# Optimization experiments

Measured on AMD Instinct MI355X. Metric: run time of the kernel, lower is better.

## Reference

```python
import jax, jax.numpy as jnp
import numpy as np

N_EXAMPLES = 10  # hardcoded repeat_interleave(10) in the source

def setup_inputs() -> dict:
    key = jax.random.key(0)
    k1, k2, k3, k4 = jax.random.split(key, 4)
    B, L, S, H = 8, 256, 512, 1024
    return {
        "output": jax.random.normal(k1, (B * N_EXAMPLES, L, H), dtype=jnp.float32),
        "context0": jax.random.normal(k2, (B * N_EXAMPLES, L, H), dtype=jnp.float32),
        "context1": jax.random.normal(k3, (B, S, H), dtype=jnp.float32),
        "mask": jnp.zeros((B * N_EXAMPLES, L), dtype=bool),
        "W_out": jax.random.normal(k4, (H, 3 * H), dtype=jnp.float32) * 0.02,
        "b_out": jnp.zeros((H,), dtype=jnp.float32),
    }

def reference(output, context0, context1, mask, W_out, b_out):
    # output, context0: [B*10, L, H]; context1: [B, S, H]
    # NOTE: in the torch source, `attn.data.masked_fill(mask, -inf)` is NOT
    # in-place and its result is discarded, so the mask has no effect on the
    # math. We reproduce that faithfully: `mask` is unused.
    del mask
    set_ctx = jnp.repeat(context1, N_EXAMPLES, axis=0)  # [B*10, S, H]
    # example-attention branch: bmm -> softmax -> bmm
    ex_attn = jax.nn.softmax(jnp.einsum('bld,bsd->bls', output, context0), axis=-1)  # [B*10, L, L]
    # set-attention branch: bmm -> softmax -> bmm
    set_attn = jax.nn.softmax(jnp.einsum('bld,bsd->bls', output, set_ctx), axis=-1)  # [B*10, L, S]
    ex_c = jnp.einsum('bls,bsd->bld', ex_attn, context0)   # [B*10, L, H]
    set_c = jnp.einsum('bls,bsd->bld', set_attn, set_ctx)  # [B*10, L, H]
    all_info = jnp.concatenate([output, ex_c, set_c], axis=-1)  # [B*10, L, 3H]
    out = jnp.tanh(jnp.einsum('blk,hk->blh', all_info, W_out) + b_out)  # [B*10, L, H]
    return (out, ex_attn, set_attn)
```

## Files before the change

kernel.cpp:

```cpp
#include <hip/hip_runtime.h>
#include <stdint.h>
#include <math.h>

typedef unsigned short u16;
typedef __attribute__((ext_vector_type(8))) short short8;
typedef __attribute__((ext_vector_type(4))) float floatx4;

__device__ __forceinline__ u16 f32_to_bf16(float f) {
    union { float f; uint32_t u; } v; v.f = f;
    uint32_t r = v.u + 0x7FFF + ((v.u >> 16) & 1);
    return (u16)(r >> 16);
}
__device__ __forceinline__ float bf16_to_f32(u16 h) {
    union { uint32_t u; float f; } v; v.u = ((uint32_t)h) << 16; return v.f;
}

__device__ __forceinline__ void gl_lds16(const u16* g, u16* l) {
    __builtin_amdgcn_global_load_lds(
        (const __attribute__((address_space(1))) void*)g,
        (__attribute__((address_space(3))) void*)l, 16, 0, 0);
}


__global__ void split_kernel(const float4* __restrict__ x, ushort4* __restrict__ hi,
                             ushort4* __restrict__ lo, long n4) {
    long i = (long)blockIdx.x * blockDim.x + threadIdx.x;
    if (i >= n4) return;
    float4 v = x[i];
    ushort4 h, l;
    h.x = f32_to_bf16(v.x); l.x = f32_to_bf16(v.x - bf16_to_f32(h.x));
    h.y = f32_to_bf16(v.y); l.y = f32_to_bf16(v.y - bf16_to_f32(h.y));
    h.z = f32_to_bf16(v.z); l.z = f32_to_bf16(v.z - bf16_to_f32(h.z));
    h.w = f32_to_bf16(v.w); l.w = f32_to_bf16(v.w - bf16_to_f32(h.w));
    hi[i] = h; lo[i] = l;
}

__global__ void conv_kernel(const float4* __restrict__ x, ushort4* __restrict__ hi, long n4) {
    long i = (long)blockIdx.x * blockDim.x + threadIdx.x;
    if (i >= n4) return;
    float4 v = x[i];
    ushort4 h;
    h.x = f32_to_bf16(v.x); h.y = f32_to_bf16(v.y);
    h.z = f32_to_bf16(v.z); h.w = f32_to_bf16(v.w);
    hi[i] = h;
}

__global__ void transpose_bf16(const float* __restrict__ src, u16* __restrict__ dst,
                               int R, int C) {
    __shared__ float tile[32][33];
    long base = (long)blockIdx.z * R * C;
    int c0 = blockIdx.x * 32, r0 = blockIdx.y * 32;
    #pragma unroll
    for (int i = threadIdx.y; i < 32; i += 8)
        tile[i][threadIdx.x] = src[base + (long)(r0 + i) * C + c0 + threadIdx.x];
    __syncthreads();
    #pragma unroll
    for (int i = threadIdx.y; i < 32; i += 8)
        dst[base + (long)(c0 + i) * R + r0 + threadIdx.x] = f32_to_bf16(tile[threadIdx.x][i]);
}

template <int VPT>
__global__ void softmax_rows(float* __restrict__ data, u16* __restrict__ outb) {
    const int SL = VPT * 64;
    int row = blockIdx.x * 4 + (threadIdx.x >> 6);
    int lane = threadIdx.x & 63;
    long base = (long)row * SL + lane;
    float v[VPT];
    #pragma unroll
    for (int i = 0; i < VPT; ++i) v[i] = data[base + i * 64];
    float m = v[0];
    #pragma unroll
    for (int i = 1; i < VPT; ++i) m = fmaxf(m, v[i]);
    #pragma unroll
    for (int off = 32; off > 0; off >>= 1) m = fmaxf(m, __shfl_xor(m, off, 64));
    float s = 0.f;
    #pragma unroll
    for (int i = 0; i < VPT; ++i) { v[i] = __expf(v[i] - m); s += v[i]; }
    #pragma unroll
    for (int off = 32; off > 0; off >>= 1) s += __shfl_xor(s, off, 64);
    float inv = 1.0f / s;
    #pragma unroll
    for (int i = 0; i < VPT; ++i) {
        float r = v[i] * inv;
        data[base + i * 64] = r;
        outb[base + i * 64] = f32_to_bf16(r);
    }
}

struct GemmP {
    const u16* A[3];
    const u16* B[3];
    long strideAb, strideBb, strideCb;
    int bdiv, nseg, Kper, lda, ldb, ldc, mode;
    float* Cf; u16* Cb; const float* bias;
};

__global__ __launch_bounds__(256) void gemm_bt(GemmP p) {
    __shared__ u16 As[128 * 64];
    __shared__ u16 Bs[128 * 64];
    const int tid  = threadIdx.x;
    const int lane = tid & 63;
    const int wave = tid >> 6;
    const int quad = lane >> 4;
    const int l15  = lane & 15;
    const int wm = (wave & 1) * 64;
    const int wn = (wave >> 1) * 64;
    const int n0 = blockIdx.x * 128;
    const int m0 = blockIdx.y * 128;
    const int bz = blockIdx.z;

    const int stg_r8 = tid >> 3;
    const int stg_c  = ((tid & 7) ^ (stg_r8 & 7)) * 8;
    const int xorl   = l15 & 7;

    floatx4 acc[4][4];
    #pragma unroll
    for (int i = 0; i < 4; ++i)
        #pragma unroll
        for (int j = 0; j < 4; ++j)
            acc[i][j] = (floatx4){0.f, 0.f, 0.f, 0.f};

    const long aoff = (long)bz * p.strideAb;
    const long boff = (long)(bz / p.bdiv) * p.strideBb;

    for (int seg = 0; seg < p.nseg; ++seg) {
        const u16* Ag = p.A[seg] + aoff + (long)m0 * p.lda;
        const u16* Bg = p.B[seg] + boff + (long)n0 * p.ldb;
        for (int k0 = 0; k0 < p.Kper; k0 += 64) {
            __syncthreads();
            #pragma unroll
            for (int i = 0; i < 4; ++i) {
                const int r = i * 32 + stg_r8;
                gl_lds16(Ag + (long)r * p.lda + k0 + stg_c, &As[(i * 256 + tid) * 8]);
            }
            #pragma unroll
            for (int i = 0; i < 4; ++i) {
                const int r = i * 32 + stg_r8;
                gl_lds16(Bg + (long)r * p.ldb + k0 + stg_c, &Bs[(i * 256 + tid) * 8]);
            }
            __syncthreads();
            #pragma unroll
            for (int kk = 0; kk < 2; ++kk) {
                const int cs = ((kk * 4 + quad) ^ xorl) * 8;
                short8 af[4], bfr[4];
                #pragma unroll
                for (int i = 0; i < 4; ++i)
                    af[i] = *(const short8*)&As[(wm + i * 16 + l15) * 64 + cs];
                #pragma unroll
                for (int i = 0; i < 4; ++i)
                    bfr[i] = *(const short8*)&Bs[(wn + i * 16 + l15) * 64 + cs];
                #pragma unroll
                for (int mi = 0; mi < 4; ++mi)
                    #pragma unroll
                    for (int ni = 0; ni < 4; ++ni)
                        acc[mi][ni] = __builtin_amdgcn_mfma_f32_16x16x32_bf16(
                            af[mi], bfr[ni], acc[mi][ni], 0, 0, 0);
            }
        }
    }

    const long coff = (long)bz * p.strideCb;
    const int rb = m0 + wm + quad * 4;
    const int cbase = n0 + wn + l15;
    if (p.mode == 2) {
        #pragma unroll
        for (int ni = 0; ni < 4; ++ni) {
            const float bv = p.bias[cbase + ni * 16];
            #pragma unroll
            for (int mi = 0; mi < 4; ++mi)
                #pragma unroll
                for (int j = 0; j < 4; ++j)
                    p.Cf[coff + (long)(rb + mi * 16 + j) * p.ldc + cbase + ni * 16] =
                        tanhf(acc[mi][ni][j] + bv);
        }
    } else if (p.mode == 0) {
        #pragma unroll
        for (int ni = 0; ni < 4; ++ni)
            #pragma unroll
            for (int mi = 0; mi < 4; ++mi)
                #pragma unroll
                for (int j = 0; j < 4; ++j)
                    p.Cf[coff + (long)(rb + mi * 16 + j) * p.ldc + cbase + ni * 16] =
                        acc[mi][ni][j];
    } else {
        #pragma unroll
        for (int ni = 0; ni < 4; ++ni)
            #pragma unroll
            for (int mi = 0; mi < 4; ++mi)
                #pragma unroll
                for (int j = 0; j < 4; ++j)
                    p.Cb[coff + (long)(rb + mi * 16 + j) * p.ldc + cbase + ni * 16] =
                        f32_to_bf16(acc[mi][ni][j]);
    }
}

extern "C" void kernel_launch(void* const* d_in, const int* in_sizes, int n_in,
                              void* d_out, int out_size, void* d_ws, size_t ws_size,
                              hipStream_t stream) {
    const int BT = 80, L = 256, S = 512, H = 1024;
    const long NO   = (long)BT * L * H;
    const long NC1  = (long)8 * S * H;
    const long NW   = (long)H * 3 * H;
    const long NEXA = (long)BT * L * L;

    const float* X    = (const float*)d_in[0];
    const float* C0   = (const float*)d_in[1];
    const float* C1   = (const float*)d_in[2];
    const float* Wf   = (const float*)d_in[4];
    const float* bias = (const float*)d_in[5];

    float* out  = (float*)d_out;
    float* exa  = out + NO;
    float* seta = exa + NEXA;

    char* wsb = (char*)d_ws;
    size_t off = 0;
    auto alloc = [&](long nbytes) -> void* {
        void* p = (void*)(wsb + off);
        off += ((size_t)nbytes + 255) & ~(size_t)255;
        return p;
    };
    u16* Xhi  = (u16*)alloc(NO * 2);
    u16* Xlo  = (u16*)alloc(NO * 2);
    u16* C0hi = (u16*)alloc(NO * 2);
    u16* C0lo = (u16*)alloc(NO * 2);
    u16* C1hi = (u16*)alloc(NC1 * 2);
    u16* C1lo = (u16*)alloc(NC1 * 2);
    u16* Wb   = (u16*)alloc(NW * 2);
    u16* exab = (u16*)alloc(NEXA * 2);
    u16* setab= (u16*)alloc((long)BT * L * S * 2);
    u16* C0T = C0lo;
    u16* C1T = C1lo;
    u16* exc = Xlo;
    u16* setc = C0hi;

    split_kernel<<<(int)(NO / 4 / 256), 256, 0, stream>>>((const float4*)X, (ushort4*)Xhi, (ushort4*)Xlo, NO / 4);
    split_kernel<<<(int)(NO / 4 / 256), 256, 0, stream>>>((const float4*)C0, (ushort4*)C0hi, (ushort4*)C0lo, NO / 4);
    split_kernel<<<(int)(NC1 / 4 / 256), 256, 0, stream>>>((const float4*)C1, (ushort4*)C1hi, (ushort4*)C1lo, NC1 / 4);
    conv_kernel<<<(int)(NW / 4 / 256), 256, 0, stream>>>((const float4*)Wf, (ushort4*)Wb, NW / 4);

    {
        GemmP p{};
        p.A[0] = Xhi;  p.A[1] = Xlo;  p.A[2] = Xhi;
        p.B[0] = C0hi; p.B[1] = C0hi; p.B[2] = C0lo;
        p.strideAb = (long)L * H; p.strideBb = (long)L * H; p.strideCb = (long)L * L;
        p.bdiv = 1; p.nseg = 3; p.Kper = H; p.lda = H; p.ldb = H; p.ldc = L; p.mode = 0;
        p.Cf = exa; p.Cb = nullptr; p.bias = nullptr;
        gemm_bt<<<dim3(L / 128, L / 128, BT), 256, 0, stream>>>(p);
    }
    softmax_rows<4><<<BT * L / 4, 256, 0, stream>>>(exa, exab);

    {
        GemmP p{};
        p.A[0] = Xhi;  p.A[1] = Xlo;  p.A[2] = Xhi;
        p.B[0] = C1hi; p.B[1] = C1hi; p.B[2] = C1lo;
        p.strideAb = (long)L * H; p.strideBb = (long)S * H; p.strideCb = (long)L * S;
        p.bdiv = 10; p.nseg = 3; p.Kper = H; p.lda = H; p.ldb = H; p.ldc = S; p.mode = 0;
        p.Cf = seta; p.Cb = nullptr; p.bias = nullptr;
        gemm_bt<<<dim3(S / 128, L / 128, BT), 256, 0, stream>>>(p);
    }
    softmax_rows<8><<<BT * L / 4, 256, 0, stream>>>(seta, setab);

    transpose_bf16<<<dim3(H / 32, L / 32, BT), dim3(32, 8), 0, stream>>>(C0, C0T, L, H);
    transpose_bf16<<<dim3(H / 32, S / 32, 8), dim3(32, 8), 0, stream>>>(C1, C1T, S, H);

    {
        GemmP p{};
        p.A[0] = exab; p.A[1] = exab; p.A[2] = exab;
        p.B[0] = C0T;  p.B[1] = C0T;  p.B[2] = C0T;
        p.strideAb = (long)L * L; p.strideBb = (long)H * L; p.strideCb = (long)L * H;
        p.bdiv = 1; p.nseg = 1; p.Kper = L; p.lda = L; p.ldb = L; p.ldc = H; p.mode = 1;
        p.Cf = nullptr; p.Cb = exc; p.bias = nullptr;
        gemm_bt<<<dim3(H / 128, L / 128, BT), 256, 0, stream>>>(p);
    }
    {
        GemmP p{};
        p.A[0] = setab; p.A[1] = setab; p.A[2] = setab;
        p.B[0] = C1T;   p.B[1] = C1T;   p.B[2] = C1T;
        p.strideAb = (long)L * S; p.strideBb = (long)H * S; p.strideCb = (long)L * H;
        p.bdiv = 10; p.nseg = 1; p.Kper = S; p.lda = S; p.ldb = S; p.ldc = H; p.mode = 1;
        p.Cf = nullptr; p.Cb = setc; p.bias = nullptr;
        gemm_bt<<<dim3(H / 128, L / 128, BT), 256, 0, stream>>>(p);
    }
    {
        GemmP p{};
        p.A[0] = Xhi; p.A[1] = exc; p.A[2] = setc;
        p.B[0] = Wb;  p.B[1] = Wb + 1024; p.B[2] = Wb + 2048;
        p.strideAb = 0; p.strideBb = 0; p.strideCb = 0;
        p.bdiv = 1; p.nseg = 3; p.Kper = H; p.lda = H; p.ldb = 3 * H; p.ldc = H; p.mode = 2;
        p.Cf = out; p.Cb = nullptr; p.bias = bias;
        gemm_bt<<<dim3(H / 128, BT * L / 128, 1), 256, 0, stream>>>(p);
    }
}
```

Before: 847.3 us.

## Split 3-pass bf16 score GEMMs across grid z and sum partials in softmax

```diff
diff --git a/kernel.cpp b/kernel.cpp
--- a/kernel.cpp
+++ b/kernel.cpp
@@ -45,9 +45,9 @@
     hi[i] = h;
 }
 
-__global__ void transpose_bf16(const float* __restrict__ src, u16* __restrict__ dst,
-                               int R, int C) {
-    __shared__ float tile[32][33];
+__global__ void transpose_u16(const u16* __restrict__ src, u16* __restrict__ dst,
+                              int R, int C) {
+    __shared__ u16 tile[32][34];
     long base = (long)blockIdx.z * R * C;
     int c0 = blockIdx.x * 32, r0 = blockIdx.y * 32;
     #pragma unroll
@@ -56,18 +56,21 @@
     __syncthreads();
     #pragma unroll
     for (int i = threadIdx.y; i < 32; i += 8)
-        dst[base + (long)(c0 + i) * R + r0 + threadIdx.x] = f32_to_bf16(tile[threadIdx.x][i]);
-}
-
-template <int VPT>
-__global__ void softmax_rows(float* __restrict__ data, u16* __restrict__ outb) {
-    const int SL = VPT * 64;
+        dst[base + (long)(c0 + i) * R + r0 + threadIdx.x] = tile[threadIdx.x][i];
+}
+
+template <int VPT, int NS>
+__global__ void softmax_rows(float* __restrict__ data, const float* __restrict__ q1,
+                             const float* __restrict__ q2, u16* __restrict__ outb) {
     int row = blockIdx.x * 4 + (threadIdx.x >> 6);
     int lane = threadIdx.x & 63;
-    long base = (long)row * SL + lane;
+    long base = (long)row * (VPT * 64) + lane;
     float v[VPT];
     #pragma unroll
-    for (int i = 0; i < VPT; ++i) v[i] = data[base + i * 64];
+    for (int i = 0; i < VPT; ++i) {
+        v[i] = data[base + i * 64];
+        if (NS == 3) v[i] += q1[base + i * 64] + q2[base + i * 64];
+    }
     float m = v[0];
     #pragma unroll
     for (int i = 1; i < VPT; ++i) m = fmaxf(m, v[i]);
@@ -90,8 +93,10 @@
 struct GemmP {
     const u16* A[3];
     const u16* B[3];
+    float* Cfs[3];
     long strideAb, strideBb, strideCb;
     int bdiv, nseg, Kper, lda, ldb, ldc, mode;
+    int zsplit, nbatch;
     float* Cf; u16* Cb; const float* bias;
 };
 
@@ -107,7 +112,16 @@
     const int wn = (wave >> 1) * 64;
     const int n0 = blockIdx.x * 128;
     const int m0 = blockIdx.y * 128;
-    const int bz = blockIdx.z;
+
+    int bz = blockIdx.z;
+    int seg0 = 0, nseg = p.nseg;
+    float* Cf = p.Cf;
+    if (p.zsplit) {
+        seg0 = bz / p.nbatch;
+        bz   = bz % p.nbatch;
+        nseg = 1;
+        Cf   = p.Cfs[seg0];
+    }
 
     const int stg_r8 = tid >> 3;
     const int stg_c  = ((tid & 7) ^ (stg_r8 & 7)) * 8;
@@ -123,7 +137,7 @@
     const long aoff = (long)bz * p.strideAb;
     const long boff = (long)(bz / p.bdiv) * p.strideBb;
 
-    for (int seg = 0; seg < p.nseg; ++seg) {
+    for (int seg = seg0; seg < seg0 + nseg; ++seg) {
         const u16* Ag = p.A[seg] + aoff + (long)m0 * p.lda;
         const u16* Bg = p.B[seg] + boff + (long)n0 * p.ldb;
         for (int k0 = 0; k0 < p.Kper; k0 += 64) {
@@ -170,7 +184,7 @@
             for (int mi = 0; mi < 4; ++mi)
                 #pragma unroll
                 for (int j = 0; j < 4; ++j)
-                    p.Cf[coff + (long)(rb + mi * 16 + j) * p.ldc + cbase + ni * 16] =
+                    Cf[coff + (long)(rb + mi * 16 + j) * p.ldc + cbase + ni * 16] =
                         tanhf(acc[mi][ni][j] + bv);
         }
     } else if (p.mode == 0) {
@@ -180,7 +194,7 @@
             for (int mi = 0; mi < 4; ++mi)
                 #pragma unroll
                 for (int j = 0; j < 4; ++j)
-                    p.Cf[coff + (long)(rb + mi * 16 + j) * p.ldc + cbase + ni * 16] =
+                    Cf[coff + (long)(rb + mi * 16 + j) * p.ldc + cbase + ni * 16] =
                         acc[mi][ni][j];
     } else {
         #pragma unroll
@@ -198,10 +212,11 @@
                               void* d_out, int out_size, void* d_ws, size_t ws_size,
                               hipStream_t stream) {
     const int BT = 80, L = 256, S = 512, H = 1024;
-    const long NO   = (long)BT * L * H;
-    const long NC1  = (long)8 * S * H;
-    const long NW   = (long)H * 3 * H;
-    const long NEXA = (long)BT * L * L;
+    const long NO    = (long)BT * L * H;
+    const long NC1   = (long)8 * S * H;
+    const long NW    = (long)H * 3 * H;
+    const long NEXA  = (long)BT * L * L;
+    const long NSETA = (long)BT * L * S;
 
     const float* X    = (const float*)d_in[0];
     const float* C0   = (const float*)d_in[1];
@@ -228,7 +243,14 @@
     u16* C1lo = (u16*)alloc(NC1 * 2);
     u16* Wb   = (u16*)alloc(NW * 2);
     u16* exab = (u16*)alloc(NEXA * 2);
-    u16* setab= (u16*)alloc((long)BT * L * S * 2);
+    u16* setab= (u16*)alloc(NSETA * 2);
+    size_t base_off = off;
+    float* P1a = (float*)alloc(NEXA * 4);
+    float* P1b = (float*)alloc(NEXA * 4);
+    float* P2b = (float*)alloc(NSETA * 4);
+    float* P2a = P1a;
+    const bool full = (off <= ws_size);
+    (void)base_off;
     u16* C0T = C0lo;
     u16* C1T = C1lo;
     u16* exc = Xlo;
@@ -245,10 +267,17 @@
         p.B[0] = C0hi; p.B[1] = C0hi; p.B[2] = C0lo;
         p.strideAb = (long)L * H; p.strideBb = (long)L * H; p.strideCb = (long)L * L;
         p.bdiv = 1; p.nseg = 3; p.Kper = H; p.lda = H; p.ldb = H; p.ldc = L; p.mode = 0;
-        p.Cf = exa; p.Cb = nullptr; p.bias = nullptr;
-        gemm_bt<<<dim3(L / 128, L / 128, BT), 256, 0, stream>>>(p);
-    }
-    softmax_rows<4><<<BT * L / 4, 256, 0, stream>>>(exa, exab);
+        if (full) {
+            p.zsplit = 1; p.nbatch = BT;
+            p.Cfs[0] = exa; p.Cfs[1] = P1a; p.Cfs[2] = P1b;
+            gemm_bt<<<dim3(L / 128, L / 128, 3 * BT), 256, 0, stream>>>(p);
+            softmax_rows<4, 3><<<BT * L / 4, 256, 0, stream>>>(exa, P1a, P1b, exab);
+        } else {
+            p.Cf = exa;
+            gemm_bt<<<dim3(L / 128, L / 128, BT), 256, 0, stream>>>(p);
+            softmax_rows<4, 1><<<BT * L / 4, 256, 0, stream>>>(exa, nullptr, nullptr, exab);
+        }
+    }
 
     {
         GemmP p{};
@@ -256,30 +285,35 @@
         p.B[0] = C1hi; p.B[1] = C1hi; p.B[2] = C1lo;
         p.strideAb = (long)L * H; p.strideBb = (long)S * H; p.strideCb = (long)L * S;
         p.bdiv = 10; p.nseg = 3; p.Kper = H; p.lda = H; p.ldb = H; p.ldc = S; p.mode = 0;
-        p.Cf = seta; p.Cb = nullptr; p.bias = nullptr;
-        gemm_bt<<<dim3(S / 128, L / 128, BT), 256, 0, stream>>>(p);
-    }
-    softmax_rows<8><<<BT * L / 4, 256, 0, stream>>>(seta, setab);
-
-    transpose_bf16<<<dim3(H / 32, L / 32, BT), dim3(32, 8), 0, stream>>>(C0, C0T, L, H);
-    transpose_bf16<<<dim3(H / 32, S / 32, 8), dim3(32, 8), 0, stream>>>(C1, C1T, S, H);
-
-    {
-        GemmP p{};
-        p.A[0] = exab; p.A[1] = exab; p.A[2] = exab;
-        p.B[0] = C0T;  p.B[1] = C0T;  p.B[2] = C0T;
+        if (full) {
+            p.zsplit = 1; p.nbatch = BT;
+            p.Cfs[0] = seta; p.Cfs[1] = P2a; p.Cfs[2] = P2b;
+            gemm_bt<<<dim3(S / 128, L / 128, 3 * BT), 256, 0, stream>>>(p);
+            softmax_rows<8, 3><<<BT * L / 4, 256, 0, stream>>>(seta, P2a, P2b, setab);
+        } else {
+            p.Cf = seta;
+            gemm_bt<<<dim3(S / 128, L / 128, BT), 256, 0, stream>>>(p);
+            softmax_rows<8, 1><<<BT * L / 4, 256, 0, stream>>>(seta, nullptr, nullptr, setab);
+        }
+    }
+
+    transpose_u16<<<dim3(H / 32, L / 32, BT), dim3(32, 8), 0, stream>>>(C0hi, C0T, L, H);
+    transpose_u16<<<dim3(H / 32, S / 32, 8), dim3(32, 8), 0, stream>>>(C1hi, C1T, S, H);
+
+    {
+        GemmP p{};
+        p.A[0] = exab; p.B[0] = C0T;
         p.strideAb = (long)L * L; p.strideBb = (long)H * L; p.strideCb = (long)L * H;
         p.bdiv = 1; p.nseg = 1; p.Kper = L; p.lda = L; p.ldb = L; p.ldc = H; p.mode = 1;
-        p.Cf = nullptr; p.Cb = exc; p.bias = nullptr;
+        p.Cb = exc;
         gemm_bt<<<dim3(H / 128, L / 128, BT), 256, 0, stream>>>(p);
     }
     {
         GemmP p{};
-        p.A[0] = setab; p.A[1] = setab; p.A[2] = setab;
-        p.B[0] = C1T;   p.B[1] = C1T;   p.B[2] = C1T;
+        p.A[0] = setab; p.B[0] = C1T;
         p.strideAb = (long)L * S; p.strideBb = (long)H * S; p.strideCb = (long)L * H;
         p.bdiv = 10; p.nseg = 1; p.Kper = S; p.lda = S; p.ldb = S; p.ldc = H; p.mode = 1;
-        p.Cf = nullptr; p.Cb = setc; p.bias = nullptr;
+        p.Cb = setc;
         gemm_bt<<<dim3(H / 128, L / 128, BT), 256, 0, stream>>>(p);
     }
     {
@@ -288,7 +322,7 @@
         p.B[0] = Wb;  p.B[1] = Wb + 1024; p.B[2] = Wb + 2048;
         p.strideAb = 0; p.strideBb = 0; p.strideCb = 0;
         p.bdiv = 1; p.nseg = 3; p.Kper = H; p.lda = H; p.ldb = 3 * H; p.ldc = H; p.mode = 2;
-        p.Cf = out; p.Cb = nullptr; p.bias = bias;
+        p.Cf = out; p.bias = bias;
         gemm_bt<<<dim3(H / 128, BT * L / 128, 1), 256, 0, stream>>>(p);
     }
 }
```

Result: slower. 864.4 us (+2.0%).

## Merge both score GEMMs into one launch, remap blocks, transpose from bf16 split

Applied to the files above, without the earlier changes.

```diff
diff --git a/kernel.cpp b/kernel.cpp
--- a/kernel.cpp
+++ b/kernel.cpp
@@ -45,9 +45,9 @@
     hi[i] = h;
 }
 
-__global__ void transpose_bf16(const float* __restrict__ src, u16* __restrict__ dst,
-                               int R, int C) {
-    __shared__ float tile[32][33];
+__global__ void transpose_u16(const u16* __restrict__ src, u16* __restrict__ dst,
+                              int R, int C) {
+    __shared__ u16 tile[32][34];
     long base = (long)blockIdx.z * R * C;
     int c0 = blockIdx.x * 32, r0 = blockIdx.y * 32;
     #pragma unroll
@@ -56,15 +56,14 @@
     __syncthreads();
     #pragma unroll
     for (int i = threadIdx.y; i < 32; i += 8)
-        dst[base + (long)(c0 + i) * R + r0 + threadIdx.x] = f32_to_bf16(tile[threadIdx.x][i]);
+        dst[base + (long)(c0 + i) * R + r0 + threadIdx.x] = tile[threadIdx.x][i];
 }
 
 template <int VPT>
 __global__ void softmax_rows(float* __restrict__ data, u16* __restrict__ outb) {
-    const int SL = VPT * 64;
     int row = blockIdx.x * 4 + (threadIdx.x >> 6);
     int lane = threadIdx.x & 63;
-    long base = (long)row * SL + lane;
+    long base = (long)row * (VPT * 64) + lane;
     float v[VPT];
     #pragma unroll
     for (int i = 0; i < VPT; ++i) v[i] = data[base + i * 64];
@@ -90,9 +89,11 @@
 struct GemmP {
     const u16* A[3];
     const u16* B[3];
-    long strideAb, strideBb, strideCb;
-    int bdiv, nseg, Kper, lda, ldb, ldc, mode;
-    float* Cf; u16* Cb; const float* bias;
+    const u16* B2[3];
+    long strideAb, strideBb, strideB2b, strideCb, strideC2b;
+    int bdiv, bdiv2, nseg, Kper, lda, ldb, ldb2, ldc, ldc2, mode;
+    int gx, gy, nx1;
+    float* Cf; float* Cf2; u16* Cb; const float* bias;
 };
 
 __global__ __launch_bounds__(256) void gemm_bt(GemmP p) {
@@ -105,9 +106,29 @@
     const int l15  = lane & 15;
     const int wm = (wave & 1) * 64;
     const int wn = (wave >> 1) * 64;
-    const int n0 = blockIdx.x * 128;
-    const int m0 = blockIdx.y * 128;
-    const int bz = blockIdx.z;
+
+    const int f  = blockIdx.x;
+    const int Tx = gridDim.x >> 3;
+    const int t  = (f & 7) * Tx + (f >> 3);
+    const int n  = t % p.gx;
+    const int r  = t / p.gx;
+    const int m0 = (r % p.gy) * 128;
+    const int bz = r / p.gy;
+
+    const u16* Bsegs[3];
+    int ldb, ldc, nn, bdv;
+    long bstr, cstr;
+    float* Cf;
+    if (n < p.nx1) {
+        Bsegs[0] = p.B[0]; Bsegs[1] = p.B[1]; Bsegs[2] = p.B[2];
+        ldb = p.ldb; ldc = p.ldc; bstr = p.strideBb; cstr = p.strideCb;
+        Cf = p.Cf; bdv = p.bdiv; nn = n;
+    } else {
+        Bsegs[0] = p.B2[0]; Bsegs[1] = p.B2[1]; Bsegs[2] = p.B2[2];
+        ldb = p.ldb2; ldc = p.ldc2; bstr = p.strideB2b; cstr = p.strideC2b;
+        Cf = p.Cf2; bdv = p.bdiv2; nn = n - p.nx1;
+    }
+    const int n0 = nn * 128;
 
     const int stg_r8 = tid >> 3;
     const int stg_c  = ((tid & 7) ^ (stg_r8 & 7)) * 8;
@@ -120,23 +141,23 @@
         for (int j = 0; j < 4; ++j)
             acc[i][j] = (floatx4){0.f, 0.f, 0.f, 0.f};
 
-    const long aoff = (long)bz * p.strideAb;
-    const long boff = (long)(bz / p.bdiv) * p.strideBb;
+    const long aoff = (long)bz * p.strideAb + (long)m0 * p.lda;
+    const long boff = (long)(bz / bdv) * bstr + (long)n0 * ldb;
 
     for (int seg = 0; seg < p.nseg; ++seg) {
-        const u16* Ag = p.A[seg] + aoff + (long)m0 * p.lda;
-        const u16* Bg = p.B[seg] + boff + (long)n0 * p.ldb;
+        const u16* Ag = p.A[seg] + aoff;
+        const u16* Bg = Bsegs[seg] + boff;
         for (int k0 = 0; k0 < p.Kper; k0 += 64) {
             __syncthreads();
             #pragma unroll
             for (int i = 0; i < 4; ++i) {
-                const int r = i * 32 + stg_r8;
-                gl_lds16(Ag + (long)r * p.lda + k0 + stg_c, &As[(i * 256 + tid) * 8]);
+                const int rr = i * 32 + stg_r8;
+                gl_lds16(Ag + (long)rr * p.lda + k0 + stg_c, &As[(i * 256 + tid) * 8]);
             }
             #pragma unroll
             for (int i = 0; i < 4; ++i) {
-                const int r = i * 32 + stg_r8;
-                gl_lds16(Bg + (long)r * p.ldb + k0 + stg_c, &Bs[(i * 256 + tid) * 8]);
+                const int rr = i * 32 + stg_r8;
+                gl_lds16(Bg + (long)rr * ldb + k0 + stg_c, &Bs[(i * 256 + tid) * 8]);
             }
             __syncthreads();
             #pragma unroll
@@ -159,7 +180,7 @@
         }
     }
 
-    const long coff = (long)bz * p.strideCb;
+    const long coff = (long)bz * cstr;
     const int rb = m0 + wm + quad * 4;
     const int cbase = n0 + wn + l15;
     if (p.mode == 2) {
@@ -170,7 +191,7 @@
             for (int mi = 0; mi < 4; ++mi)
                 #pragma unroll
                 for (int j = 0; j < 4; ++j)
-                    p.Cf[coff + (long)(rb + mi * 16 + j) * p.ldc + cbase + ni * 16] =
+                    Cf[coff + (long)(rb + mi * 16 + j) * ldc + cbase + ni * 16] =
                         tanhf(acc[mi][ni][j] + bv);
         }
     } else if (p.mode == 0) {
@@ -180,7 +201,7 @@
             for (int mi = 0; mi < 4; ++mi)
                 #pragma unroll
                 for (int j = 0; j < 4; ++j)
-                    p.Cf[coff + (long)(rb + mi * 16 + j) * p.ldc + cbase + ni * 16] =
+                    Cf[coff + (long)(rb + mi * 16 + j) * ldc + cbase + ni * 16] =
                         acc[mi][ni][j];
     } else {
         #pragma unroll
@@ -189,7 +210,7 @@
             for (int mi = 0; mi < 4; ++mi)
                 #pragma unroll
                 for (int j = 0; j < 4; ++j)
-                    p.Cb[coff + (long)(rb + mi * 16 + j) * p.ldc + cbase + ni * 16] =
+                    p.Cb[coff + (long)(rb + mi * 16 + j) * ldc + cbase + ni * 16] =
                         f32_to_bf16(acc[mi][ni][j]);
     }
 }
@@ -198,10 +219,11 @@
                               void* d_out, int out_size, void* d_ws, size_t ws_size,
                               hipStream_t stream) {
     const int BT = 80, L = 256, S = 512, H = 1024;
-    const long NO   = (long)BT * L * H;
-    const long NC1  = (long)8 * S * H;
-    const long NW   = (long)H * 3 * H;
-    const long NEXA = (long)BT * L * L;
+    const long NO    = (long)BT * L * H;
+    const long NC1   = (long)8 * S * H;
+    const long NW    = (long)H * 3 * H;
+    const long NEXA  = (long)BT * L * L;
+    const long NSETA = (long)BT * L * S;
 
     const float* X    = (const float*)d_in[0];
     const float* C0   = (const float*)d_in[1];
@@ -228,7 +250,7 @@
     u16* C1lo = (u16*)alloc(NC1 * 2);
     u16* Wb   = (u16*)alloc(NW * 2);
     u16* exab = (u16*)alloc(NEXA * 2);
-    u16* setab= (u16*)alloc((long)BT * L * S * 2);
+    u16* setab= (u16*)alloc(NSETA * 2);
     u16* C0T = C0lo;
     u16* C1T = C1lo;
     u16* exc = Xlo;
@@ -242,45 +264,41 @@
     {
         GemmP p{};
         p.A[0] = Xhi;  p.A[1] = Xlo;  p.A[2] = Xhi;
-        p.B[0] = C0hi; p.B[1] = C0hi; p.B[2] = C0lo;
-        p.strideAb = (long)L * H; p.strideBb = (long)L * H; p.strideCb = (long)L * L;
-        p.bdiv = 1; p.nseg = 3; p.Kper = H; p.lda = H; p.ldb = H; p.ldc = L; p.mode = 0;
-        p.Cf = exa; p.Cb = nullptr; p.bias = nullptr;
-        gemm_bt<<<dim3(L / 128, L / 128, BT), 256, 0, stream>>>(p);
+        p.B[0]  = C0hi; p.B[1]  = C0hi; p.B[2]  = C0lo;
+        p.B2[0] = C1hi; p.B2[1] = C1hi; p.B2[2] = C1lo;
+        p.strideAb = (long)L * H;
+        p.strideBb = (long)L * H;  p.strideB2b = (long)S * H;
+        p.strideCb = (long)L * L;  p.strideC2b = (long)L * S;
+        p.bdiv = 1; p.bdiv2 = 10;
+        p.nseg = 3; p.Kper = H; p.lda = H; p.ldb = H; p.ldb2 = H;
+        p.ldc = L; p.ldc2 = S; p.mode = 0;
+        p.gx = 6; p.gy = 2; p.nx1 = 2;
+        p.Cf = exa; p.Cf2 = seta;
+        gemm_bt<<<dim3(6 * 2 * BT, 1, 1), 256, 0, stream>>>(p);
     }
     softmax_rows<4><<<BT * L / 4, 256, 0, stream>>>(exa, exab);
+    softmax_rows<8><<<BT * L / 4, 256, 0, stream>>>(seta, setab);
+
+    transpose_u16<<<dim3(H / 32, L / 32, BT), dim3(32, 8), 0, stream>>>(C0hi, C0T, L, H);
+    transpose_u16<<<dim3(H / 32, S / 32, 8), dim3(32, 8), 0, stream>>>(C1hi, C1T, S, H);
 
     {
         GemmP p{};
-        p.A[0] = Xhi;  p.A[1] = Xlo;  p.A[2] = Xhi;
-        p.B[0] = C1hi; p.B[1] = C1hi; p.B[2] = C1lo;
-        p.strideAb = (long)L * H; p.strideBb = (long)S * H; p.strideCb = (long)L * S;
-        p.bdiv = 10; p.nseg = 3; p.Kper = H; p.lda = H; p.ldb = H; p.ldc = S; p.mode = 0;
-        p.Cf = seta; p.Cb = nullptr; p.bias = nullptr;
-        gemm_bt<<<dim3(S / 128, L / 128, BT), 256, 0, stream>>>(p);
-    }
-    softmax_rows<8><<<BT * L / 4, 256, 0, stream>>>(seta, setab);
-
-    transpose_bf16<<<dim3(H / 32, L / 32, BT), dim3(32, 8), 0, stream>>>(C0, C0T, L, H);
-    transpose_bf16<<<dim3(H / 32, S / 32, 8), dim3(32, 8), 0, stream>>>(C1, C1T, S, H);
-
+        p.A[0] = exab; p.B[0] = C0T;
+        p.strideAb = (long)L * L; p.strideBb = (long)H * L; p.strideCb = (long)L * H;
+        p.bdiv = 1; p.nseg = 1; p.Kper = L; p.lda = L; p.ldb = L; p.ldc = H; p.mode = 1;
+        p.gx = 8; p.gy = 2; p.nx1 = 8;
+        p.Cb = exc;
+        gemm_bt<<<dim3(8 * 2 * BT, 1, 1), 256, 0, stream>>>(p);
+    }
     {
         GemmP p{};
-        p.A[0] = exab; p.A[1] = exab; p.A[2] = exab;
-        p.B[0] = C0T;  p.B[1] = C0T;  p.B[2] = C0T;
-        p.strideAb = (long)L * L; p.strideBb = (long)H * L; p.strideCb = (long)L * H;
-        p.bdiv = 1; p.nseg = 1; p.Kper = L; p.lda = L; p.ldb = L; p.ldc = H; p.mode = 1;
-        p.Cf = nullptr; p.Cb = exc; p.bias = nullptr;
-        gemm_bt<<<dim3(H / 128, L / 128, BT), 256, 0, stream>>>(p);
-    }
-    {
-        GemmP p{};
-        p.A[0] = setab; p.A[1] = setab; p.A[2] = setab;
-        p.B[0] = C1T;   p.B[1] = C1T;   p.B[2] = C1T;
+        p.A[0] = setab; p.B[0] = C1T;
         p.strideAb = (long)L * S; p.strideBb = (long)H * S; p.strideCb = (long)L * H;
         p.bdiv = 10; p.nseg = 1; p.Kper = S; p.lda = S; p.ldb = S; p.ldc = H; p.mode = 1;
-        p.Cf = nullptr; p.Cb = setc; p.bias = nullptr;
-        gemm_bt<<<dim3(H / 128, L / 128, BT), 256, 0, stream>>>(p);
+        p.gx = 8; p.gy = 2; p.nx1 = 8;
+        p.Cb = setc;
+        gemm_bt<<<dim3(8 * 2 * BT, 1, 1), 256, 0, stream>>>(p);
     }
     {
         GemmP p{};
@@ -288,7 +306,8 @@
         p.B[0] = Wb;  p.B[1] = Wb + 1024; p.B[2] = Wb + 2048;
         p.strideAb = 0; p.strideBb = 0; p.strideCb = 0;
         p.bdiv = 1; p.nseg = 3; p.Kper = H; p.lda = H; p.ldb = 3 * H; p.ldc = H; p.mode = 2;
-        p.Cf = out; p.Cb = nullptr; p.bias = bias;
-        gemm_bt<<<dim3(H / 128, BT * L / 128, 1), 256, 0, stream>>>(p);
-    }
-}
+        p.gx = 8; p.gy = BT * L / 128; p.nx1 = 8;
+        p.Cf = out; p.bias = bias;
+        gemm_bt<<<dim3(8 * (BT * L / 128), 1, 1), 256, 0, stream>>>(p);
+    }
+}
```

Measured after the change: 766.7 us. 9.5% less time.
